# Kernel tuning notes

Hardware: AMD Instinct MI355X
Metric: run time of the kernel (lower is better)

Reference implementation:

```python
import jax, jax.numpy as jnp
import numpy as np

N_HEAD = 16


def setup_inputs() -> dict:
    key = jax.random.key(0)
    ks = jax.random.split(key, 5)
    B, T, C = 4, 2048, 1024
    s = 1.0 / np.sqrt(C)
    x = jax.random.normal(ks[0], (B, T, C), dtype=jnp.float32)
    wq = jax.random.normal(ks[1], (C, C), dtype=jnp.float32) * s
    wk = jax.random.normal(ks[2], (C, C), dtype=jnp.float32) * s
    wv = jax.random.normal(ks[3], (C, C), dtype=jnp.float32) * s
    wo = jax.random.normal(ks[4], (C, C), dtype=jnp.float32) * s
    return {"x": x, "wq": wq, "wk": wk, "wv": wv, "wo": wo}


def _attn(x, wq, wk, wv, wo):
    B, T, C = x.shape
    H = N_HEAD
    D = C // H
    scale = 1.0 / np.sqrt(D)
    # nn.Linear(x) = x @ W.T; weights stored as [out, in]
    q = (x @ wq.T).reshape(B, T, H, D).transpose(0, 2, 1, 3)  # [B,H,T,D]
    k = (x @ wk.T).reshape(B, T, H, D).transpose(0, 2, 1, 3)
    v = (x @ wv.T).reshape(B, T, H, D).transpose(0, 2, 1, 3)
    scores = jnp.einsum("bhtd,bhsd->bhts", q, k) * scale  # [B,H,T,T]
    mask = jnp.triu(jnp.full((T, T), -jnp.inf, dtype=scores.dtype), k=1)
    attn = jax.nn.softmax(scores + mask, axis=-1)
    out = jnp.einsum("bhts,bhsd->bhtd", attn, v)  # [B,H,T,D]
    out = out.transpose(0, 2, 1, 3).reshape(B, T, C)
    return out @ wo.T


def reference(x, wq, wk, wv, wo):
    return _attn(x, wq, wk, wv, wo)
```

## Files before the change

kernel.cpp:

```cpp
#include <hip/hip_runtime.h>

typedef __bf16 bf16x8 __attribute__((ext_vector_type(8)));
typedef float f32x4 __attribute__((ext_vector_type(4)));
typedef unsigned short ushortx8 __attribute__((ext_vector_type(8)));
typedef unsigned short ushortx4 __attribute__((ext_vector_type(4)));

#if __has_builtin(__builtin_amdgcn_exp2f)
#define EXP2F(x) __builtin_amdgcn_exp2f(x)
#else
#define EXP2F(x) exp2f(x)
#endif
#if __has_builtin(__builtin_amdgcn_rcpf)
#define RCPF(x) __builtin_amdgcn_rcpf(x)
#else
#define RCPF(x) (1.0f / (x))
#endif

__device__ __forceinline__ unsigned short f2bf(float f) {
    unsigned int u = __builtin_bit_cast(unsigned int, f);
    u += 0x7fffu + ((u >> 16) & 1u);
    return (unsigned short)(u >> 16);
}

__device__ __forceinline__ bf16x8 ld_frag(const unsigned short* p) {
    return __builtin_bit_cast(bf16x8, *(const ushortx8*)p);
}

__device__ __forceinline__ unsigned int pack_bf2(float lo, float hi) {
#if __has_builtin(__builtin_amdgcn_cvt_pk_bf16_f32)
    typedef __bf16 bf16x2 __attribute__((ext_vector_type(2)));
    bf16x2 v = __builtin_amdgcn_cvt_pk_bf16_f32(lo, hi);
    return __builtin_bit_cast(unsigned int, v);
#else
    unsigned int ulo = __builtin_bit_cast(unsigned int, lo) + 0x8000u;
    unsigned int uhi = __builtin_bit_cast(unsigned int, hi) + 0x8000u;
    return __builtin_amdgcn_perm(uhi, ulo, 0x07060302u);
#endif
}

__device__ __forceinline__ void async_cp16(const unsigned short* g, unsigned short* l) {
    __builtin_amdgcn_global_load_lds(
        (const __attribute__((address_space(1))) unsigned int*)g,
        (__attribute__((address_space(3))) unsigned int*)(unsigned long)(unsigned long long)(uintptr_t)
            reinterpret_cast<uintptr_t>(l),
        16, 0, 0);
}

__global__ void cvt_all_kernel(const float* __restrict__ x,
                               const float* __restrict__ wq, const float* __restrict__ wk,
                               const float* __restrict__ wv, const float* __restrict__ wo,
                               unsigned short* __restrict__ xb,
                               unsigned short* __restrict__ wqb) {
    const int NX4 = (8192 * 1024) / 4;
    int i = blockIdx.x * blockDim.x + threadIdx.x;
    if (i < NX4) {
        float4 f = ((const float4*)x)[i];
        ushortx4 u = { f2bf(f.x), f2bf(f.y), f2bf(f.z), f2bf(f.w) };
        ((ushortx4*)xb)[i] = u;
    } else {
        int k = i - NX4;
        int w = k >> 18;
        int r = k & 0x3FFFF;
        const float* src = (w == 0) ? wq : (w == 1) ? wk : (w == 2) ? wv : wo;
        float4 f = ((const float4*)src)[r];
        ushortx4 u = { f2bf(f.x), f2bf(f.y), f2bf(f.z), f2bf(f.w) };
        ((ushortx4*)wqb)[k] = u;
    }
}

__global__ __launch_bounds__(256, 3) void qkv_gemm(
    const unsigned short* __restrict__ xb,
    const unsigned short* __restrict__ wqb,
    const unsigned short* __restrict__ wkb,
    const unsigned short* __restrict__ wvb,
    unsigned short* __restrict__ q_ws,
    unsigned short* __restrict__ k_ws,
    unsigned short* __restrict__ v_ws)
{
    __shared__ __align__(16) unsigned short A_lds[128 * 64];
    __shared__ __align__(16) unsigned short B_lds[128 * 64];

    const int tid = threadIdx.x;
    const int wv = tid >> 6;
    const int lane = tid & 63;
    const int quad = lane >> 4;
    const int l15 = lane & 15;
    const int wm = wv >> 1;
    const int wn = wv & 1;

    const int m0 = blockIdx.x * 128;
    const int mat = blockIdx.y >> 3;
    const int n0 = (blockIdx.y & 7) * 128;
    const unsigned short* wb = (mat == 0) ? wqb : (mat == 1 ? wkb : wvb);

    const int srow8 = lane >> 3;
    const int scol8 = ((lane & 7) ^ srow8) * 8;
    const unsigned short* ag0 = xb + (size_t)(m0 + wv * 32 + srow8) * 1024 + scol8;
    const unsigned short* bg0 = wb + (size_t)(n0 + wv * 32 + srow8) * 1024 + scol8;
    unsigned short* la0 = A_lds + (wv * 32) * 64;
    unsigned short* lb0 = B_lds + (wv * 32) * 64;

    const int swz = (l15 & 7);

    f32x4 acc[4][4] = {};

    for (int kt = 0; kt < 1024; kt += 64) {
        __syncthreads();
#pragma unroll
        for (int i = 0; i < 4; ++i) {
            async_cp16(ag0 + kt + i * (8 * 1024), la0 + i * (8 * 64));
            async_cp16(bg0 + kt + i * (8 * 1024), lb0 + i * (8 * 64));
        }
        __builtin_amdgcn_s_waitcnt(0x0F70);
        __syncthreads();

#pragma unroll
        for (int kk = 0; kk < 2; ++kk) {
            bf16x8 af[4], bf[4];
#pragma unroll
            for (int i = 0; i < 4; ++i)
                af[i] = ld_frag(A_lds + (wm * 64 + i * 16 + l15) * 64 + (((kk * 4 + quad) ^ swz) * 8));
#pragma unroll
            for (int i = 0; i < 4; ++i)
                bf[i] = ld_frag(B_lds + (wn * 64 + i * 16 + l15) * 64 + (((kk * 4 + quad) ^ swz) * 8));
#pragma unroll
            for (int i = 0; i < 4; ++i)
#pragma unroll
                for (int j = 0; j < 4; ++j)
                    acc[i][j] = __builtin_amdgcn_mfma_f32_16x16x32_bf16(af[i], bf[j], acc[i][j], 0, 0, 0);
        }
    }

    const float qscale = 0.125f * 1.4426950408889634f;
    const int mbase = m0 + wm * 64;
    const int nbase = n0 + wn * 64;
#pragma unroll
    for (int i = 0; i < 4; ++i) {
        const int mrow = mbase + i * 16 + quad * 4;
        const int b = mrow >> 11;
        const int trow = mrow & 2047;
#pragma unroll
        for (int j = 0; j < 4; ++j) {
            const int nloc = nbase + j * 16 + l15;
            const int h = nloc >> 6, d = nloc & 63;
            if (mat == 2) {
                ushortx4 pk = { f2bf(acc[i][j][0]), f2bf(acc[i][j][1]),
                                f2bf(acc[i][j][2]), f2bf(acc[i][j][3]) };
                *(ushortx4*)&v_ws[(((size_t)(b * 16 + h)) * 64 + d) * 2048 + trow] = pk;
            } else {
                unsigned short* dst = (mat == 0) ? q_ws : k_ws;
                float sc = (mat == 0) ? qscale : 1.0f;
                size_t base = (((size_t)(b * 16 + h)) * 2048 + trow) * 64 + d;
                dst[base]       = f2bf(acc[i][j][0] * sc);
                dst[base + 64]  = f2bf(acc[i][j][1] * sc);
                dst[base + 128] = f2bf(acc[i][j][2] * sc);
                dst[base + 192] = f2bf(acc[i][j][3] * sc);
            }
        }
    }
}

__global__ __launch_bounds__(256, 2) void attn_kernel(
    const unsigned short* __restrict__ q_ws,
    const unsigned short* __restrict__ k_ws,
    const unsigned short* __restrict__ v_ws,
    unsigned short* __restrict__ o_ws)
{
    __shared__ __align__(16) unsigned short K_lds[128][72];
    __shared__ __align__(16) unsigned short Vt_lds[64][136];
    __shared__ __align__(16) unsigned short P_lds[128][136];

    const int tid = threadIdx.x;
    const int wvid = tid >> 6, lane = tid & 63, quad = lane >> 4, l15 = lane & 15;
    const int bh = blockIdx.x;
    const int b = bh >> 4, h = bh & 15;
    const int bt = 15 - (int)blockIdx.y;
    const int t0 = bt * 128;

    const unsigned short* qb = q_ws + (size_t)bh * 2048 * 64;
    const unsigned short* kb = k_ws + (size_t)bh * 2048 * 64;
    const unsigned short* vb = v_ws + (size_t)bh * 64 * 2048;

    ushortx8 ones_u = { 0x3F80, 0x3F80, 0x3F80, 0x3F80, 0x3F80, 0x3F80, 0x3F80, 0x3F80 };
    const bf16x8 ones = __builtin_bit_cast(bf16x8, ones_u);

    bf16x8 bq[2][2];
#pragma unroll
    for (int it = 0; it < 2; ++it)
#pragma unroll
        for (int kk = 0; kk < 2; ++kk)
            bq[it][kk] = ld_frag(qb + (size_t)(t0 + wvid * 32 + it * 16 + l15) * 64 + kk * 32 + quad * 8);

    f32x4 acc_o[2][4] = {};
    f32x4 l_acc[2] = {};

    const int kr = tid >> 1, kc = (tid & 1) * 32;
    const int vr = tid >> 2, vc = (tid & 3) * 32;

    ushortx8 kvr[4], vvr[4];
#pragma unroll
    for (int u = 0; u < 4; ++u)
        kvr[u] = *(const ushortx8*)(kb + (size_t)kr * 64 + kc + u * 8);
#pragma unroll
    for (int u = 0; u < 4; ++u)
        vvr[u] = *(const ushortx8*)(vb + (size_t)vr * 2048 + vc + u * 8);

    for (int j = 0; j <= bt; ++j) {
        __syncthreads();
#pragma unroll
        for (int u = 0; u < 4; ++u) *(ushortx8*)&K_lds[kr][kc + u * 8] = kvr[u];
#pragma unroll
        for (int u = 0; u < 4; ++u) *(ushortx8*)&Vt_lds[vr][vc + u * 8] = vvr[u];
        __syncthreads();

        if (j < bt) {
            const int s1 = (j + 1) * 128;
#pragma unroll
            for (int u = 0; u < 4; ++u)
                kvr[u] = *(const ushortx8*)(kb + (size_t)(s1 + kr) * 64 + kc + u * 8);
#pragma unroll
            for (int u = 0; u < 4; ++u)
                vvr[u] = *(const ushortx8*)(vb + (size_t)vr * 2048 + s1 + vc + u * 8);
        }

        f32x4 sacc[2][8] = {};
        __builtin_amdgcn_s_setprio(1);
#pragma unroll
        for (int is = 0; is < 8; ++is) {
            bf16x8 k0 = ld_frag(&K_lds[is * 16 + l15][quad * 8]);
            bf16x8 k1 = ld_frag(&K_lds[is * 16 + l15][32 + quad * 8]);
            sacc[0][is] = __builtin_amdgcn_mfma_f32_16x16x32_bf16(k0, bq[0][0], sacc[0][is], 0, 0, 0);
            sacc[0][is] = __builtin_amdgcn_mfma_f32_16x16x32_bf16(k1, bq[0][1], sacc[0][is], 0, 0, 0);
            sacc[1][is] = __builtin_amdgcn_mfma_f32_16x16x32_bf16(k0, bq[1][0], sacc[1][is], 0, 0, 0);
            sacc[1][is] = __builtin_amdgcn_mfma_f32_16x16x32_bf16(k1, bq[1][1], sacc[1][is], 0, 0, 0);
        }
        __builtin_amdgcn_s_setprio(0);

        if (j == bt) {
#pragma unroll
            for (int it = 0; it < 2; ++it) {
                const int tl = wvid * 32 + it * 16 + l15;
#pragma unroll
                for (int is = 0; is < 8; ++is)
#pragma unroll
                    for (int r = 0; r < 4; ++r) {
                        const int sl = is * 16 + quad * 4 + r;
                        if (sl > tl) sacc[it][is][r] = -1.0e30f;
                    }
            }
        }

#pragma unroll
        for (int it = 0; it < 2; ++it) {
            const int row = wvid * 32 + it * 16 + l15;
#pragma unroll
            for (int is = 0; is < 8; ++is) {
                float p0 = EXP2F(sacc[it][is][0]);
                float p1 = EXP2F(sacc[it][is][1]);
                float p2 = EXP2F(sacc[it][is][2]);
                float p3 = EXP2F(sacc[it][is][3]);
                uint2 pk = { pack_bf2(p0, p1), pack_bf2(p2, p3) };
                *(uint2*)&P_lds[row][is * 16 + quad * 4] = pk;
            }
        }

        asm volatile("s_waitcnt lgkmcnt(0)" ::: "memory");
        __builtin_amdgcn_sched_barrier(0);

#pragma unroll
        for (int kk = 0; kk < 4; ++kk) {
            bf16x8 p0 = ld_frag(&P_lds[wvid * 32 + l15][kk * 32 + quad * 8]);
            bf16x8 p1 = ld_frag(&P_lds[wvid * 32 + 16 + l15][kk * 32 + quad * 8]);
            __builtin_amdgcn_s_setprio(1);
            l_acc[0] = __builtin_amdgcn_mfma_f32_16x16x32_bf16(p0, ones, l_acc[0], 0, 0, 0);
            l_acc[1] = __builtin_amdgcn_mfma_f32_16x16x32_bf16(p1, ones, l_acc[1], 0, 0, 0);
#pragma unroll
            for (int id = 0; id < 4; ++id) {
                bf16x8 bv = ld_frag(&Vt_lds[id * 16 + l15][kk * 32 + quad * 8]);
                acc_o[0][id] = __builtin_amdgcn_mfma_f32_16x16x32_bf16(p0, bv, acc_o[0][id], 0, 0, 0);
                acc_o[1][id] = __builtin_amdgcn_mfma_f32_16x16x32_bf16(p1, bv, acc_o[1][id], 0, 0, 0);
            }
            __builtin_amdgcn_s_setprio(0);
        }
    }

#pragma unroll
    for (int it = 0; it < 2; ++it) {
        f32x4 rinv;
#pragma unroll
        for (int r = 0; r < 4; ++r) rinv[r] = RCPF(l_acc[it][r]);
#pragma unroll
        for (int id = 0; id < 4; ++id)
#pragma unroll
            for (int r = 0; r < 4; ++r) {
                int tg = t0 + wvid * 32 + it * 16 + quad * 4 + r;
                int c = h * 64 + id * 16 + l15;
                o_ws[(size_t)(b * 2048 + tg) * 1024 + c] = f2bf(acc_o[it][id][r] * rinv[r]);
            }
    }
}

__global__ __launch_bounds__(256, 3) void out_gemm(
    const unsigned short* __restrict__ ob,
    const unsigned short* __restrict__ wob,
    float* __restrict__ out)
{
    __shared__ __align__(16) unsigned short A_lds[128 * 64];
    __shared__ __align__(16) unsigned short B_lds[128 * 64];

    const int tid = threadIdx.x;
    const int wv = tid >> 6;
    const int lane = tid & 63;
    const int quad = lane >> 4;
    const int l15 = lane & 15;
    const int wm = wv >> 1;
    const int wn = wv & 1;

    const int m0 = blockIdx.x * 128;
    const int n0 = blockIdx.y * 128;

    const int srow8 = lane >> 3;
    const int scol8 = ((lane & 7) ^ srow8) * 8;
    const unsigned short* ag0 = ob + (size_t)(m0 + wv * 32 + srow8) * 1024 + scol8;
    const unsigned short* bg0 = wob + (size_t)(n0 + wv * 32 + srow8) * 1024 + scol8;
    unsigned short* la0 = A_lds + (wv * 32) * 64;
    unsigned short* lb0 = B_lds + (wv * 32) * 64;

    const int swz = (l15 & 7);

    f32x4 acc[4][4] = {};

    for (int kt = 0; kt < 1024; kt += 64) {
        __syncthreads();
#pragma unroll
        for (int i = 0; i < 4; ++i) {
            async_cp16(ag0 + kt + i * (8 * 1024), la0 + i * (8 * 64));
            async_cp16(bg0 + kt + i * (8 * 1024), lb0 + i * (8 * 64));
        }
        __builtin_amdgcn_s_waitcnt(0x0F70);
        __syncthreads();

#pragma unroll
        for (int kk = 0; kk < 2; ++kk) {
            bf16x8 af[4], bf[4];
#pragma unroll
            for (int i = 0; i < 4; ++i)
                af[i] = ld_frag(A_lds + (wm * 64 + i * 16 + l15) * 64 + (((kk * 4 + quad) ^ swz) * 8));
#pragma unroll
            for (int i = 0; i < 4; ++i)
                bf[i] = ld_frag(B_lds + (wn * 64 + i * 16 + l15) * 64 + (((kk * 4 + quad) ^ swz) * 8));
#pragma unroll
            for (int i = 0; i < 4; ++i)
#pragma unroll
                for (int j = 0; j < 4; ++j)
                    acc[i][j] = __builtin_amdgcn_mfma_f32_16x16x32_bf16(af[i], bf[j], acc[i][j], 0, 0, 0);
        }
    }

    const int mbase = m0 + wm * 64;
    const int nbase = n0 + wn * 64;
#pragma unroll
    for (int i = 0; i < 4; ++i) {
        const int mrow = mbase + i * 16 + quad * 4;
#pragma unroll
        for (int j = 0; j < 4; ++j) {
            const int ncol = nbase + j * 16 + l15;
            float* dst = out + (size_t)mrow * 1024 + ncol;
            dst[0]        = acc[i][j][0];
            dst[1024]     = acc[i][j][1];
            dst[2048]     = acc[i][j][2];
            dst[3072]     = acc[i][j][3];
        }
    }
}

extern "C" void kernel_launch(void* const* d_in, const int* in_sizes, int n_in,
                              void* d_out, int out_size, void* d_ws, size_t ws_size,
                              hipStream_t stream) {
    const float* x  = (const float*)d_in[0];
    const float* wq = (const float*)d_in[1];
    const float* wk = (const float*)d_in[2];
    const float* wv = (const float*)d_in[3];
    const float* wo = (const float*)d_in[4];
    float* out = (float*)d_out;

    unsigned short* ws = (unsigned short*)d_ws;
    unsigned short* xb   = ws;
    unsigned short* wqb  = xb  + (size_t)8192 * 1024;
    unsigned short* wkb  = wqb + (size_t)1024 * 1024;
    unsigned short* wvb  = wkb + (size_t)1024 * 1024;
    unsigned short* wob  = wvb + (size_t)1024 * 1024;
    unsigned short* q_ws = wob + (size_t)1024 * 1024;
    unsigned short* k_ws = q_ws + (size_t)8192 * 1024;
    unsigned short* v_ws = k_ws + (size_t)8192 * 1024;
    unsigned short* o_ws = v_ws + (size_t)8192 * 1024;

    int total4 = (8192 * 1024 + 4 * 1024 * 1024) / 4;
    cvt_all_kernel<<<(total4 + 255) / 256, 256, 0, stream>>>(x, wq, wk, wv, wo, xb, wqb);

    qkv_gemm<<<dim3(64, 24), 256, 0, stream>>>(xb, wqb, wkb, wvb, q_ws, k_ws, v_ws);
    attn_kernel<<<dim3(64, 16), 256, 0, stream>>>(q_ws, k_ws, v_ws, o_ws);
    out_gemm<<<dim3(64, 8), 256, 0, stream>>>(o_ws, wob, out);
}
```

Measured before the change: 233.6 us.

## Rewrite QKV GEMM as 256x256 tile, 8-wave, double-buffered async pipeline

Replaces the 128x128, 4-wave QKV projection GEMM with a 256x256 tile computed by 8 waves. Global-to-LDS async copies are double-buffered in 32-wide K halves so the next tile loads while MFMAs run, and MFMA sections run under raised wave priority. This aims to cut per-tile synchronisation stalls and raise operand reuse. The cost is a grid of only 384 blocks, which may leave compute units idle, plus higher register and LDS pressure.

Measured after the change: 239.6 us. 1.03x slower.

```diff
diff --git a/kernel.cpp b/kernel.cpp
--- a/kernel.cpp
+++ b/kernel.cpp
@@ -68,7 +68,7 @@
     }
 }
 
-__global__ __launch_bounds__(256, 3) void qkv_gemm(
+__global__ __launch_bounds__(512, 2) void qkv_gemm8(
     const unsigned short* __restrict__ xb,
     const unsigned short* __restrict__ wqb,
     const unsigned short* __restrict__ wkb,
@@ -77,84 +77,155 @@
     unsigned short* __restrict__ k_ws,
     unsigned short* __restrict__ v_ws)
 {
-    __shared__ __align__(16) unsigned short A_lds[128 * 64];
-    __shared__ __align__(16) unsigned short B_lds[128 * 64];
+    __shared__ __align__(16) unsigned short A_lds[2][2][256 * 32];
+    __shared__ __align__(16) unsigned short B_lds[2][2][256 * 32];
 
     const int tid = threadIdx.x;
-    const int wv = tid >> 6;
+    const int w = tid >> 6;
     const int lane = tid & 63;
     const int quad = lane >> 4;
     const int l15 = lane & 15;
-    const int wm = wv >> 1;
-    const int wn = wv & 1;
-
-    const int m0 = blockIdx.x * 128;
-    const int mat = blockIdx.y >> 3;
-    const int n0 = (blockIdx.y & 7) * 128;
+    const int wm = w >> 2;
+    const int wn = w & 3;
+
+    const int m0 = blockIdx.x * 256;
+    const int mat = blockIdx.y >> 2;
+    const int n0 = (blockIdx.y & 3) * 256;
     const unsigned short* wb = (mat == 0) ? wqb : (mat == 1 ? wkb : wvb);
 
-    const int srow8 = lane >> 3;
-    const int scol8 = ((lane & 7) ^ srow8) * 8;
-    const unsigned short* ag0 = xb + (size_t)(m0 + wv * 32 + srow8) * 1024 + scol8;
-    const unsigned short* bg0 = wb + (size_t)(n0 + wv * 32 + srow8) * 1024 + scol8;
-    unsigned short* la0 = A_lds + (wv * 32) * 64;
-    unsigned short* lb0 = B_lds + (wv * 32) * 64;
-
-    const int swz = (l15 & 7);
-
-    f32x4 acc[4][4] = {};
-
-    for (int kt = 0; kt < 1024; kt += 64) {
-        __syncthreads();
-#pragma unroll
-        for (int i = 0; i < 4; ++i) {
-            async_cp16(ag0 + kt + i * (8 * 1024), la0 + i * (8 * 64));
-            async_cp16(bg0 + kt + i * (8 * 1024), lb0 + i * (8 * 64));
-        }
-        __builtin_amdgcn_s_waitcnt(0x0F70);
-        __syncthreads();
-
-#pragma unroll
-        for (int kk = 0; kk < 2; ++kk) {
-            bf16x8 af[4], bf[4];
-#pragma unroll
-            for (int i = 0; i < 4; ++i)
-                af[i] = ld_frag(A_lds + (wm * 64 + i * 16 + l15) * 64 + (((kk * 4 + quad) ^ swz) * 8));
-#pragma unroll
-            for (int i = 0; i < 4; ++i)
-                bf[i] = ld_frag(B_lds + (wn * 64 + i * 16 + l15) * 64 + (((kk * 4 + quad) ^ swz) * 8));
-#pragma unroll
-            for (int i = 0; i < 4; ++i)
-#pragma unroll
-                for (int j = 0; j < 4; ++j)
-                    acc[i][j] = __builtin_amdgcn_mfma_f32_16x16x32_bf16(af[i], bf[j], acc[i][j], 0, 0, 0);
-        }
-    }
+    const int srow = w * 16 + (lane >> 2);
+    const int scol = ((lane & 3) ^ ((lane >> 2) & 3)) * 8;
+    const unsigned short* agA = xb + (size_t)(m0 + srow) * 1024 + scol;
+    const unsigned short* bgB = wb + (size_t)(n0 + srow) * 1024 + scol;
+    const int ldst0 = (w * 16) * 32;
+    const int ldst1 = (128 + w * 16) * 32;
+
+    const int rsw = (quad ^ (l15 & 3)) * 8;
+    const int Ar0 = (wm * 128 + l15) * 32 + rsw;
+    const int Br0 = (wn * 64 + l15) * 32 + rsw;
+
+    f32x4 acc[8][4] = {};
+
+#define STAGE_A(bufb, kh, kt)                                                   \
+    do {                                                                        \
+        async_cp16(agA + (kt) + (kh) * 32, &A_lds[bufb][kh][ldst0]);            \
+        async_cp16(agA + (size_t)128 * 1024 + (kt) + (kh) * 32, &A_lds[bufb][kh][ldst1]); \
+    } while (0)
+#define STAGE_B(bufb, kh, kt)                                                   \
+    do {                                                                        \
+        async_cp16(bgB + (kt) + (kh) * 32, &B_lds[bufb][kh][ldst0]);            \
+        async_cp16(bgB + (size_t)128 * 1024 + (kt) + (kh) * 32, &B_lds[bufb][kh][ldst1]); \
+    } while (0)
+
+    STAGE_A(0, 0, 0);
+    STAGE_B(0, 0, 0);
+    STAGE_A(0, 1, 0);
+    STAGE_B(0, 1, 0);
+
+    for (int t = 0; t < 16; ++t) {
+        const int buf = t & 1, nxt = buf ^ 1;
+        const int ktn = (t + 1) * 64;
+
+        asm volatile("s_waitcnt vmcnt(4)" ::: "memory");
+        __builtin_amdgcn_sched_barrier(0);
+        __builtin_amdgcn_s_barrier();
+        __builtin_amdgcn_sched_barrier(0);
+
+        if (t < 15) STAGE_A(nxt, 0, ktn);
+        bf16x8 af[8];
+#pragma unroll
+        for (int m = 0; m < 8; ++m)
+            af[m] = ld_frag(&A_lds[buf][0][Ar0 + m * 512]);
+        {
+            bf16x8 b0 = ld_frag(&B_lds[buf][0][Br0]);
+            bf16x8 b1 = ld_frag(&B_lds[buf][0][Br0 + 512]);
+            __builtin_amdgcn_s_setprio(1);
+#pragma unroll
+            for (int m = 0; m < 8; ++m) {
+                acc[m][0] = __builtin_amdgcn_mfma_f32_16x16x32_bf16(af[m], b0, acc[m][0], 0, 0, 0);
+                acc[m][1] = __builtin_amdgcn_mfma_f32_16x16x32_bf16(af[m], b1, acc[m][1], 0, 0, 0);
+            }
+            __builtin_amdgcn_s_setprio(0);
+        }
+
+        if (t < 15) STAGE_B(nxt, 0, ktn);
+        {
+            bf16x8 b2 = ld_frag(&B_lds[buf][0][Br0 + 1024]);
+            bf16x8 b3 = ld_frag(&B_lds[buf][0][Br0 + 1536]);
+            __builtin_amdgcn_s_setprio(1);
+#pragma unroll
+            for (int m = 0; m < 8; ++m) {
+                acc[m][2] = __builtin_amdgcn_mfma_f32_16x16x32_bf16(af[m], b2, acc[m][2], 0, 0, 0);
+                acc[m][3] = __builtin_amdgcn_mfma_f32_16x16x32_bf16(af[m], b3, acc[m][3], 0, 0, 0);
+            }
+            __builtin_amdgcn_s_setprio(0);
+        }
+
+        if (t < 15) {
+            asm volatile("s_waitcnt vmcnt(4)" ::: "memory");
+        } else {
+            asm volatile("s_waitcnt vmcnt(0)" ::: "memory");
+        }
+        __builtin_amdgcn_sched_barrier(0);
+        __builtin_amdgcn_s_barrier();
+        __builtin_amdgcn_sched_barrier(0);
+
+        if (t < 15) STAGE_A(nxt, 1, ktn);
+#pragma unroll
+        for (int m = 0; m < 8; ++m)
+            af[m] = ld_frag(&A_lds[buf][1][Ar0 + m * 512]);
+        {
+            bf16x8 b0 = ld_frag(&B_lds[buf][1][Br0]);
+            bf16x8 b1 = ld_frag(&B_lds[buf][1][Br0 + 512]);
+            __builtin_amdgcn_s_setprio(1);
+#pragma unroll
+            for (int m = 0; m < 8; ++m) {
+                acc[m][0] = __builtin_amdgcn_mfma_f32_16x16x32_bf16(af[m], b0, acc[m][0], 0, 0, 0);
+                acc[m][1] = __builtin_amdgcn_mfma_f32_16x16x32_bf16(af[m], b1, acc[m][1], 0, 0, 0);
+            }
+            __builtin_amdgcn_s_setprio(0);
+        }
+
+        if (t < 15) STAGE_B(nxt, 1, ktn);
+        {
+            bf16x8 b2 = ld_frag(&B_lds[buf][1][Br0 + 1024]);
+            bf16x8 b3 = ld_frag(&B_lds[buf][1][Br0 + 1536]);
+            __builtin_amdgcn_s_setprio(1);
+#pragma unroll
+            for (int m = 0; m < 8; ++m) {
+                acc[m][2] = __builtin_amdgcn_mfma_f32_16x16x32_bf16(af[m], b2, acc[m][2], 0, 0, 0);
+                acc[m][3] = __builtin_amdgcn_mfma_f32_16x16x32_bf16(af[m], b3, acc[m][3], 0, 0, 0);
+            }
+            __builtin_amdgcn_s_setprio(0);
+        }
+    }
+#undef STAGE_A
+#undef STAGE_B
 
     const float qscale = 0.125f * 1.4426950408889634f;
-    const int mbase = m0 + wm * 64;
+    const int mbase = m0 + wm * 128;
     const int nbase = n0 + wn * 64;
 #pragma unroll
-    for (int i = 0; i < 4; ++i) {
-        const int mrow = mbase + i * 16 + quad * 4;
+    for (int m = 0; m < 8; ++m) {
+        const int mrow = mbase + m * 16 + quad * 4;
         const int b = mrow >> 11;
         const int trow = mrow & 2047;
 #pragma unroll
-        for (int j = 0; j < 4; ++j) {
-            const int nloc = nbase + j * 16 + l15;
+        for (int n = 0; n < 4; ++n) {
+            const int nloc = nbase + n * 16 + l15;
             const int h = nloc >> 6, d = nloc & 63;
             if (mat == 2) {
-                ushortx4 pk = { f2bf(acc[i][j][0]), f2bf(acc[i][j][1]),
-                                f2bf(acc[i][j][2]), f2bf(acc[i][j][3]) };
+                ushortx4 pk = { f2bf(acc[m][n][0]), f2bf(acc[m][n][1]),
+                                f2bf(acc[m][n][2]), f2bf(acc[m][n][3]) };
                 *(ushortx4*)&v_ws[(((size_t)(b * 16 + h)) * 64 + d) * 2048 + trow] = pk;
             } else {
                 unsigned short* dst = (mat == 0) ? q_ws : k_ws;
                 float sc = (mat == 0) ? qscale : 1.0f;
                 size_t base = (((size_t)(b * 16 + h)) * 2048 + trow) * 64 + d;
-                dst[base]       = f2bf(acc[i][j][0] * sc);
-                dst[base + 64]  = f2bf(acc[i][j][1] * sc);
-                dst[base + 128] = f2bf(acc[i][j][2] * sc);
-                dst[base + 192] = f2bf(acc[i][j][3] * sc);
+                dst[base]       = f2bf(acc[m][n][0] * sc);
+                dst[base + 64]  = f2bf(acc[m][n][1] * sc);
+                dst[base + 128] = f2bf(acc[m][n][2] * sc);
+                dst[base + 192] = f2bf(acc[m][n][3] * sc);
             }
         }
     }
@@ -398,7 +469,7 @@
     int total4 = (8192 * 1024 + 4 * 1024 * 1024) / 4;
     cvt_all_kernel<<<(total4 + 255) / 256, 256, 0, stream>>>(x, wq, wk, wv, wo, xb, wqb);
 
-    qkv_gemm<<<dim3(64, 24), 256, 0, stream>>>(xb, wqb, wkb, wvb, q_ws, k_ws, v_ws);
+    qkv_gemm8<<<dim3(32, 12), 512, 0, stream>>>(xb, wqb, wkb, wvb, q_ws, k_ws, v_ws);
     attn_kernel<<<dim3(64, 16), 256, 0, stream>>>(q_ws, k_ws, v_ws, o_ws);
     out_gemm<<<dim3(64, 8), 256, 0, stream>>>(o_ws, wob, out);
 }
```
